# Optimization experiments

Measured on AMD Instinct MI355X. Metric: run time of the kernel, lower is better.

The kernel has to match this reference:

```python
import jax, jax.numpy as jnp
import numpy as np

B, D, K, NCLS, BANK = 1024, 256, 8, 71, 32


def setup_inputs() -> dict:
    key = jax.random.key(0)
    ks = jax.random.split(key, 8)
    p = lambda k: jax.random.normal(k, (D, D), jnp.float32) * 0.02  # trunc_normal std=0.02 approx
    z = jnp.zeros((D,), jnp.float32)
    return {
        "target_token": jax.random.normal(ks[0], (B, D), jnp.float32),
        "fea_bank": jax.random.normal(ks[1], (NCLS, BANK, D), jnp.float32),
        "W_e1": p(ks[2]), "b_e1": z,
        "W_o1": p(ks[3]), "b_o1": z,
        "W_e2": p(ks[4]), "b_e2": z,
        "W_o2": p(ks[5]), "b_o2": z,
        "W_f1": p(ks[6]),
        "W_f2": p(ks[7]),
    }


def reference(target_token, fea_bank, W_e1, b_e1, W_o1, b_o1,
              W_e2, b_e2, W_o2, b_o2, W_f1, W_f2):
    lin = lambda x, W, b: x @ W.T + b  # torch nn.Linear convention

    # class-mean bank and euclidean cdist [B, NCLS]
    fea_mean = fea_bank.mean(axis=1)                              # [C, D]
    d2 = (jnp.sum(target_token ** 2, -1, keepdims=True)
          - 2.0 * target_token @ fea_mean.T
          + jnp.sum(fea_mean ** 2, -1))
    dist = jnp.sqrt(jnp.maximum(d2, 0.0))
    _, idx = jax.lax.top_k(-dist, K)                              # k smallest -> [B, K]

    # stage 1: blend with nearest class means
    nearest_means = fea_mean[idx]                                 # [B, K, D]
    e1 = jax.nn.gelu(lin(nearest_means - target_token[:, None], W_e1, b_e1),
                     approximate=False)
    w1 = e1 @ W_f1.T
    e1 = e1 * jax.nn.softmax(w1, axis=1)                          # softmax over K
    off1 = jnp.tanh(lin(target_token[:, None] + e1, W_o1, b_o1))
    s1 = (1.0 + off1) * target_token[:, None]                     # [B, K, D]

    # stage 2: blend with full intra-class banks of selected classes
    feats = fea_bank[idx]                                         # [B, K, BANK, D]
    e2 = jax.nn.gelu(lin(feats - s1[:, :, None], W_e2, b_e2), approximate=False)
    w2 = e2 @ W_f2.T
    e2 = e2 * jax.nn.softmax(w2, axis=2)                          # softmax over BANK
    off2 = jnp.tanh(lin(s1[:, :, None] + e2, W_o2, b_o2))
    s2 = ((1.0 + off2) * s1[:, :, None]).sum(axis=2)              # [B, K, D]

    return (s1, s2)
```

## Files before the change

kernel.cpp:

```cpp
#include <hip/hip_runtime.h>
#include <hip/hip_bf16.h>

#define BB 1024
#define DD 256
#define KK 8
#define NCLS_ 71
#define BANK_ 32
#define BKROWS (BB*KK)
#define NBROWS (NCLS_*BANK_)

typedef __bf16 bf16x8 __attribute__((ext_vector_type(8)));
typedef __bf16 bf16x4 __attribute__((ext_vector_type(4)));
typedef float f32x4 __attribute__((ext_vector_type(4)));

__device__ __forceinline__ float gelu_fast(float x) {
    float z = __expf(-1.702f * x);
    return x * __builtin_amdgcn_rcpf(1.0f + z);
}
__device__ __forceinline__ float tanh_fast(float y) {
    float z = __expf(2.0f * y);
    return 1.0f - 2.0f * __builtin_amdgcn_rcpf(z + 1.0f);
}
__device__ __forceinline__ int swz(int row, int colByte) {
    return (row * 512 + colByte) ^ ((row & 7) << 4);
}

template<int MT, int NT>
__device__ __forceinline__ void gemm_tile(const __bf16* __restrict__ Wg,
                                          const char* Ab, int m_base, int n_base,
                                          int lane, f32x4 (&acc)[MT][NT])
{
    #pragma unroll
    for (int ks = 0; ks < 8; ++ks) {
        bf16x8 a[MT];
        #pragma unroll
        for (int mt = 0; mt < MT; ++mt) {
            int row = m_base + mt*16 + (lane & 15);
            int cb  = ks*64 + ((lane >> 4) << 4);
            a[mt] = *reinterpret_cast<const bf16x8*>(Ab + swz(row, cb));
        }
        #pragma unroll
        for (int nt = 0; nt < NT; ++nt) {
            int n  = n_base + nt*16 + (lane & 15);
            int k0 = ks*32 + ((lane >> 4) << 3);
            bf16x8 b = *reinterpret_cast<const bf16x8*>(Wg + n*DD + k0);
            #pragma unroll
            for (int mt = 0; mt < MT; ++mt)
                acc[mt][nt] = __builtin_amdgcn_mfma_f32_16x16x32_bf16(a[mt], b, acc[mt][nt], 0, 0, 0);
        }
    }
}

__global__ __launch_bounds__(256) void k_prep(
    const float* __restrict__ We1f, const float* __restrict__ Wo1f,
    const float* __restrict__ We2f, const float* __restrict__ Wo2f,
    const float* __restrict__ Wf1f, const float* __restrict__ Wf2f,
    const float* __restrict__ fb,
    __bf16* __restrict__ We1, __bf16* __restrict__ Wo1,
    __bf16* __restrict__ We2, __bf16* __restrict__ Wo2,
    __bf16* __restrict__ Wf1, __bf16* __restrict__ Wf2,
    __bf16* __restrict__ fbb, float* __restrict__ fmean)
{
    int b = blockIdx.x, tid = threadIdx.x;
    if (b < 384) {
        int w = b >> 6;
        const float* s; __bf16* d;
        switch (w) {
            case 0: s = We1f; d = We1; break;
            case 1: s = Wo1f; d = Wo1; break;
            case 2: s = We2f; d = We2; break;
            case 3: s = Wo2f; d = Wo2; break;
            case 4: s = Wf1f; d = Wf1; break;
            default: s = Wf2f; d = Wf2; break;
        }
        int i = (b & 63)*256 + tid;
        float4 v = reinterpret_cast<const float4*>(s)[i];
        bf16x4 o = {(__bf16)v.x, (__bf16)v.y, (__bf16)v.z, (__bf16)v.w};
        *reinterpret_cast<bf16x4*>(d + i*4) = o;
    } else if (b < 952) {
        int i = (b - 384)*256 + tid;
        float4 v = reinterpret_cast<const float4*>(fb)[i];
        bf16x4 o = {(__bf16)v.x, (__bf16)v.y, (__bf16)v.z, (__bf16)v.w};
        *reinterpret_cast<bf16x4*>(fbb + i*4) = o;
    } else {
        int c = b - 952, d = tid;
        float s = 0.f;
        #pragma unroll
        for (int j = 0; j < BANK_; ++j) s += fb[(c*BANK_ + j)*DD + d];
        fmean[c*DD + d] = s * (1.0f / BANK_);
    }
}

__global__ __launch_bounds__(64) void k_topk(const float* __restrict__ tgt,
                                             const float* __restrict__ fmean,
                                             int* __restrict__ idx) {
    __shared__ float d2s[NCLS_];
    int b = blockIdx.x, l = threadIdx.x;
    float t0 = tgt[b*DD + l],       t1 = tgt[b*DD + 64 + l];
    float t2 = tgt[b*DD + 128 + l], t3 = tgt[b*DD + 192 + l];
    for (int c = 0; c < NCLS_; ++c) {
        const float* m = fmean + c*DD;
        float a0 = t0 - m[l], a1 = t1 - m[64+l], a2 = t2 - m[128+l], a3 = t3 - m[192+l];
        float p = a0*a0 + a1*a1 + a2*a2 + a3*a3;
        #pragma unroll
        for (int o = 32; o > 0; o >>= 1) p += __shfl_xor(p, o);
        if (l == 0) d2s[c] = p;
    }
    if (l == 0) {
        for (int t = 0; t < KK; ++t) {
            float best = 3.4e38f; int bi = 0;
            for (int c = 0; c < NCLS_; ++c) { float v = d2s[c]; if (v < best) { best = v; bi = c; } }
            d2s[bi] = 3.4e38f;
            idx[b*KK + t] = bi;
        }
    }
}

__global__ __launch_bounds__(128) void k_stage1(
    const float* __restrict__ tgt, const float* __restrict__ fmean, const int* __restrict__ idx,
    const __bf16* __restrict__ We1, const float* __restrict__ be1,
    const __bf16* __restrict__ Wf1,
    const __bf16* __restrict__ Wo1, const float* __restrict__ bo1,
    float* __restrict__ out_s1, __bf16* __restrict__ s1b)
{
    __shared__ __bf16 As[16*256];
    __shared__ float tl[256];
    __shared__ int cls[8];
    char* Ab = (char*)As;
    int tid = threadIdx.x, lane = tid & 63, wid = tid >> 6;
    int b = blockIdx.x;
    if (tid < 8) cls[tid] = idx[b*KK + tid];
    if (tid < 64) reinterpret_cast<float4*>(tl)[tid] = reinterpret_cast<const float4*>(tgt + b*DD)[tid];
    {
        uint4 zz = {0u,0u,0u,0u};
        #pragma unroll
        for (int i = 0; i < 2; ++i) {
            int f = i*128 + tid;
            int row = 8 + (f >> 5), c = f & 31;
            *reinterpret_cast<uint4*>(Ab + swz(row, c*16)) = zz;
        }
    }
    __syncthreads();
    int c16 = tid & 31, q = tid >> 5;
    #pragma unroll
    for (int i = 0; i < 2; ++i) {
        int row = i*4 + q;
        const float* mb = fmean + cls[row]*DD + c16*8;
        const float* tb = tl + c16*8;
        float4 m0 = *(const float4*)mb, m1 = *(const float4*)(mb+4);
        float4 t0 = *(const float4*)tb, t1 = *(const float4*)(tb+4);
        bf16x8 o = {(__bf16)(m0.x-t0.x), (__bf16)(m0.y-t0.y), (__bf16)(m0.z-t0.z), (__bf16)(m0.w-t0.w),
                    (__bf16)(m1.x-t1.x), (__bf16)(m1.y-t1.y), (__bf16)(m1.z-t1.z), (__bf16)(m1.w-t1.w)};
        *reinterpret_cast<bf16x8*>(Ab + swz(row, c16*16)) = o;
    }
    __syncthreads();
    int n_base = wid * 128;
    int qr = lane >> 4;
    const f32x4 z = {0.f, 0.f, 0.f, 0.f};
    f32x4 acc[1][8];
    #pragma unroll
    for (int nt = 0; nt < 8; ++nt) acc[0][nt] = z;
    gemm_tile<1,8>(We1, Ab, 0, n_base, lane, acc);
    float e1reg[8][4];
    #pragma unroll
    for (int nt = 0; nt < 8; ++nt)
        #pragma unroll
        for (int r = 0; r < 4; ++r) {
            int col = n_base + nt*16 + (lane & 15);
            e1reg[nt][r] = gelu_fast(acc[0][nt][r] + be1[col]);
        }
    __syncthreads();
    if (qr < 2)
        #pragma unroll
        for (int nt = 0; nt < 8; ++nt)
            #pragma unroll
            for (int r = 0; r < 4; ++r) {
                int row = qr*4 + r;
                int col = n_base + nt*16 + (lane & 15);
                *(__bf16*)(Ab + swz(row, col*2)) = (__bf16)e1reg[nt][r];
            }
    __syncthreads();
    f32x4 acc2[1][8];
    #pragma unroll
    for (int nt = 0; nt < 8; ++nt) acc2[0][nt] = z;
    gemm_tile<1,8>(Wf1, Ab, 0, n_base, lane, acc2);
    float a2v[8][4];
    #pragma unroll
    for (int nt = 0; nt < 8; ++nt) {
        float mx = fmaxf(fmaxf(acc2[0][nt][0], acc2[0][nt][1]),
                         fmaxf(acc2[0][nt][2], acc2[0][nt][3]));
        mx = fmaxf(mx, __shfl_xor(mx, 16));
        float p[4], s = 0.f;
        #pragma unroll
        for (int r = 0; r < 4; ++r) { p[r] = __expf(acc2[0][nt][r] - mx); s += p[r]; }
        s += __shfl_xor(s, 16);
        float inv = __builtin_amdgcn_rcpf(s);
        int col = n_base + nt*16 + (lane & 15);
        #pragma unroll
        for (int r = 0; r < 4; ++r)
            a2v[nt][r] = tl[col] + e1reg[nt][r] * p[r] * inv;
    }
    __syncthreads();
    if (qr < 2)
        #pragma unroll
        for (int nt = 0; nt < 8; ++nt)
            #pragma unroll
            for (int r = 0; r < 4; ++r) {
                int row = qr*4 + r;
                int col = n_base + nt*16 + (lane & 15);
                *(__bf16*)(Ab + swz(row, col*2)) = (__bf16)a2v[nt][r];
            }
    __syncthreads();
    #pragma unroll
    for (int nt = 0; nt < 8; ++nt) acc[0][nt] = z;
    gemm_tile<1,8>(Wo1, Ab, 0, n_base, lane, acc);
    if (qr < 2)
        #pragma unroll
        for (int nt = 0; nt < 8; ++nt)
            #pragma unroll
            for (int r = 0; r < 4; ++r) {
                int row = qr*4 + r;
                int col = n_base + nt*16 + (lane & 15);
                float off = tanh_fast(acc[0][nt][r] + bo1[col]);
                float s1v = (1.0f + off) * tl[col];
                int g = (b*8 + row)*DD + col;
                out_s1[g] = s1v;
                s1b[g] = (__bf16)s1v;
            }
}

__global__ __launch_bounds__(256) void k_gemms(
    const __bf16* __restrict__ fbb, const __bf16* __restrict__ s1b,
    const __bf16* __restrict__ We2, const __bf16* __restrict__ Wo2,
    const float* __restrict__ be2, const float* __restrict__ bo2,
    float* __restrict__ FBe2b, float* __restrict__ S1We2, float* __restrict__ S1Wo2)
{
    __shared__ __bf16 As[64*256];
    char* Ab = (char*)As;
    int tid = threadIdx.x, lane = tid & 63, wid = tid >> 6;
    bool fbpath = blockIdx.x < 36;
    const __bf16* A = fbpath ? fbb : s1b;
    int m0 = fbpath ? blockIdx.x * 64 : (blockIdx.x - 36) * 64;
    int M  = fbpath ? NBROWS : BKROWS;
    #pragma unroll
    for (int i = 0; i < 8; ++i) {
        int f = i*256 + tid;
        int row = f >> 5, c16 = f & 31;
        uint4 v = {0u,0u,0u,0u};
        if (m0 + row < M) v = *reinterpret_cast<const uint4*>(A + (size_t)(m0+row)*DD + c16*8);
        *reinterpret_cast<uint4*>(Ab + swz(row, c16*16)) = v;
    }
    __syncthreads();
    int m_base = (wid >> 1) * 32, n_base = (wid & 1) * 128;
    const f32x4 z = {0.f, 0.f, 0.f, 0.f};
    f32x4 acc[2][8];
    #pragma unroll
    for (int mt = 0; mt < 2; ++mt)
        #pragma unroll
        for (int nt = 0; nt < 8; ++nt) acc[mt][nt] = z;
    gemm_tile<2,8>(We2, Ab, m_base, n_base, lane, acc);
    #pragma unroll
    for (int mt = 0; mt < 2; ++mt)
        #pragma unroll
        for (int nt = 0; nt < 8; ++nt)
            #pragma unroll
            for (int r = 0; r < 4; ++r) {
                int row = m_base + mt*16 + ((lane >> 4) << 2) + r;
                int col = n_base + nt*16 + (lane & 15);
                if (m0 + row < M) {
                    if (fbpath) FBe2b[(size_t)(m0+row)*DD + col] = acc[mt][nt][r] + be2[col];
                    else        S1We2[(size_t)(m0+row)*DD + col] = acc[mt][nt][r];
                }
            }
    if (!fbpath) {
        #pragma unroll
        for (int mt = 0; mt < 2; ++mt)
            #pragma unroll
            for (int nt = 0; nt < 8; ++nt) acc[mt][nt] = z;
        gemm_tile<2,8>(Wo2, Ab, m_base, n_base, lane, acc);
        #pragma unroll
        for (int mt = 0; mt < 2; ++mt)
            #pragma unroll
            for (int nt = 0; nt < 8; ++nt)
                #pragma unroll
                for (int r = 0; r < 4; ++r) {
                    int row = m_base + mt*16 + ((lane >> 4) << 2) + r;
                    int col = n_base + nt*16 + (lane & 15);
                    S1Wo2[(size_t)(m0+row)*DD + col] = acc[mt][nt][r] + bo2[col];
                }
    }
}

__global__ __launch_bounds__(512, 4) void k_stage2(
    const int* __restrict__ idx,
    const float* __restrict__ FBe2b,
    const float* __restrict__ S1We2,
    const float* __restrict__ S1Wo2,
    const __bf16* __restrict__ Wf2,
    const __bf16* __restrict__ Wo2,
    const float* __restrict__ s1,
    float* __restrict__ s2)
{
    __shared__ __bf16 As[128*256];
    __shared__ int clss[4];
    char* Ab = (char*)As;
    int tid = threadIdx.x, lane = tid & 63, wid = tid >> 6;
    int u0 = blockIdx.x * 4;
    if (tid < 4) clss[tid] = idx[u0 + tid];
    __syncthreads();
    int c16 = tid & 31, q = tid >> 5;
    #pragma unroll
    for (int i = 0; i < 8; ++i) {
        int row = i*16 + q;
        int unit = row >> 5, j = row & 31;
        const float* fbp = FBe2b + ((size_t)clss[unit]*BANK_ + j)*DD + c16*8;
        const float* sbp = S1We2 + (size_t)(u0+unit)*DD + c16*8;
        float4 f0 = *(const float4*)fbp, f1 = *(const float4*)(fbp+4);
        float4 g0 = *(const float4*)sbp, g1 = *(const float4*)(sbp+4);
        bf16x8 o = {(__bf16)gelu_fast(f0.x-g0.x), (__bf16)gelu_fast(f0.y-g0.y),
                    (__bf16)gelu_fast(f0.z-g0.z), (__bf16)gelu_fast(f0.w-g0.w),
                    (__bf16)gelu_fast(f1.x-g1.x), (__bf16)gelu_fast(f1.y-g1.y),
                    (__bf16)gelu_fast(f1.z-g1.z), (__bf16)gelu_fast(f1.w-g1.w)};
        *reinterpret_cast<bf16x8*>(Ab + swz(row, c16*16)) = o;
    }
    __syncthreads();
    int n_base = wid * 32;
    const f32x4 z = {0.f, 0.f, 0.f, 0.f};
    f32x4 acc[8][2];
    #pragma unroll
    for (int mt = 0; mt < 8; ++mt)
        #pragma unroll
        for (int nt = 0; nt < 2; ++nt) acc[mt][nt] = z;
    gemm_tile<8,2>(Wf2, Ab, 0, n_base, lane, acc);
    float inv_[4][2];
    #pragma unroll
    for (int unit = 0; unit < 4; ++unit)
        #pragma unroll
        for (int nt = 0; nt < 2; ++nt) {
            float mx = -3.4e38f;
            #pragma unroll
            for (int mh = 0; mh < 2; ++mh)
                #pragma unroll
                for (int r = 0; r < 4; ++r) mx = fmaxf(mx, acc[unit*2+mh][nt][r]);
            mx = fmaxf(mx, __shfl_xor(mx, 16));
            mx = fmaxf(mx, __shfl_xor(mx, 32));
            float s = 0.f;
            #pragma unroll
            for (int mh = 0; mh < 2; ++mh)
                #pragma unroll
                for (int r = 0; r < 4; ++r) {
                    float e = __expf(acc[unit*2+mh][nt][r] - mx);
                    acc[unit*2+mh][nt][r] = e;
                    s += e;
                }
            s += __shfl_xor(s, 16);
            s += __shfl_xor(s, 32);
            inv_[unit][nt] = __builtin_amdgcn_rcpf(s);
        }
    __syncthreads();
    #pragma unroll
    for (int mt = 0; mt < 8; ++mt)
        #pragma unroll
        for (int nt = 0; nt < 2; ++nt)
            #pragma unroll
            for (int r = 0; r < 4; ++r) {
                int row = mt*16 + ((lane >> 4) << 2) + r;
                int col = n_base + nt*16 + (lane & 15);
                __bf16* p16 = (__bf16*)(Ab + swz(row, col*2));
                *p16 = (__bf16)((float)*p16 * acc[mt][nt][r] * inv_[mt>>1][nt]);
            }
    __syncthreads();
    #pragma unroll
    for (int mt = 0; mt < 8; ++mt)
        #pragma unroll
        for (int nt = 0; nt < 2; ++nt) acc[mt][nt] = z;
    gemm_tile<8,2>(Wo2, Ab, 0, n_base, lane, acc);
    #pragma unroll
    for (int unit = 0; unit < 4; ++unit) {
        size_t u = u0 + unit;
        #pragma unroll
        for (int nt = 0; nt < 2; ++nt) {
            int col = n_base + nt*16 + (lane & 15);
            float srow = S1Wo2[u*DD + col];
            float cs = 0.f;
            #pragma unroll
            for (int mh = 0; mh < 2; ++mh)
                #pragma unroll
                for (int r = 0; r < 4; ++r) cs += tanh_fast(acc[unit*2+mh][nt][r] + srow);
            cs += __shfl_xor(cs, 16);
            cs += __shfl_xor(cs, 32);
            if ((lane >> 4) == 0)
                s2[u*DD + col] = s1[u*DD + col] * (32.0f + cs);
        }
    }
}

extern "C" void kernel_launch(void* const* d_in, const int* in_sizes, int n_in,
                              void* d_out, int out_size, void* d_ws, size_t ws_size,
                              hipStream_t stream)
{
    const float* tgt  = (const float*)d_in[0];
    const float* fb   = (const float*)d_in[1];
    const float* We1f = (const float*)d_in[2];
    const float* be1  = (const float*)d_in[3];
    const float* Wo1f = (const float*)d_in[4];
    const float* bo1  = (const float*)d_in[5];
    const float* We2f = (const float*)d_in[6];
    const float* be2  = (const float*)d_in[7];
    const float* Wo2f = (const float*)d_in[8];
    const float* bo2  = (const float*)d_in[9];
    const float* Wf1f = (const float*)d_in[10];
    const float* Wf2f = (const float*)d_in[11];

    char* ws = (char*)d_ws;
    size_t off = 0;
    auto alloc = [&](size_t bytes) { char* p = ws + off; off += (bytes + 255) & ~255ull; return p; };
    float*  fmean = (float*)alloc(NCLS_*DD*4);
    int*    idx   = (int*)alloc(BB*KK*4);
    __bf16* We1   = (__bf16*)alloc(DD*DD*2);
    __bf16* Wo1   = (__bf16*)alloc(DD*DD*2);
    __bf16* We2   = (__bf16*)alloc(DD*DD*2);
    __bf16* Wo2   = (__bf16*)alloc(DD*DD*2);
    __bf16* Wf1   = (__bf16*)alloc(DD*DD*2);
    __bf16* Wf2   = (__bf16*)alloc(DD*DD*2);
    __bf16* fbb   = (__bf16*)alloc((size_t)NBROWS*DD*2);
    __bf16* s1b   = (__bf16*)alloc((size_t)BKROWS*DD*2);
    float*  FBe2b = (float*)alloc((size_t)NBROWS*DD*4);
    float*  S1We2 = (float*)alloc((size_t)BKROWS*DD*4);
    float*  S1Wo2 = (float*)alloc((size_t)BKROWS*DD*4);

    float* out_s1 = (float*)d_out;
    float* out_s2 = out_s1 + (size_t)BKROWS*DD;

    k_prep<<<1023, 256, 0, stream>>>(We1f, Wo1f, We2f, Wo2f, Wf1f, Wf2f, fb,
                                     We1, Wo1, We2, Wo2, Wf1, Wf2, fbb, fmean);
    k_topk<<<BB, 64, 0, stream>>>(tgt, fmean, idx);
    k_stage1<<<BB, 128, 0, stream>>>(tgt, fmean, idx, We1, be1, Wf1, Wo1, bo1, out_s1, s1b);
    k_gemms<<<36 + BKROWS/64, 256, 0, stream>>>(fbb, s1b, We2, Wo2, be2, bo2,
                                                FBe2b, S1We2, S1Wo2);
    k_stage2<<<BKROWS/4, 512, 0, stream>>>(idx, FBe2b, S1We2, S1Wo2, Wf2, Wo2, out_s1, out_s2);
}
```

Before: 300.9 us.

## Fuse top-k into stage1, store intermediates as bf16, shrink gemm and stage2 tiles

```diff
diff --git a/kernel.cpp b/kernel.cpp
--- a/kernel.cpp
+++ b/kernel.cpp
@@ -91,53 +91,54 @@
     }
 }
 
-__global__ __launch_bounds__(64) void k_topk(const float* __restrict__ tgt,
-                                             const float* __restrict__ fmean,
-                                             int* __restrict__ idx) {
-    __shared__ float d2s[NCLS_];
-    int b = blockIdx.x, l = threadIdx.x;
-    float t0 = tgt[b*DD + l],       t1 = tgt[b*DD + 64 + l];
-    float t2 = tgt[b*DD + 128 + l], t3 = tgt[b*DD + 192 + l];
-    for (int c = 0; c < NCLS_; ++c) {
-        const float* m = fmean + c*DD;
-        float a0 = t0 - m[l], a1 = t1 - m[64+l], a2 = t2 - m[128+l], a3 = t3 - m[192+l];
-        float p = a0*a0 + a1*a1 + a2*a2 + a3*a3;
-        #pragma unroll
-        for (int o = 32; o > 0; o >>= 1) p += __shfl_xor(p, o);
-        if (l == 0) d2s[c] = p;
-    }
-    if (l == 0) {
+__global__ __launch_bounds__(128) void k_stage1(
+    const float* __restrict__ tgt, const float* __restrict__ fmean,
+    int* __restrict__ idxg,
+    const __bf16* __restrict__ We1, const float* __restrict__ be1,
+    const __bf16* __restrict__ Wf1,
+    const __bf16* __restrict__ Wo1, const float* __restrict__ bo1,
+    float* __restrict__ out_s1, __bf16* __restrict__ s1b)
+{
+    __shared__ __bf16 As[16*256];
+    __shared__ float tl[256];
+    __shared__ float d2s[NCLS_ + 1];
+    __shared__ int cls[8];
+    char* Ab = (char*)As;
+    int tid = threadIdx.x, lane = tid & 63, wid = tid >> 6;
+    int b = blockIdx.x;
+    if (tid < 64) reinterpret_cast<float4*>(tl)[tid] = reinterpret_cast<const float4*>(tgt + b*DD)[tid];
+    {
+        uint4 zz = {0u,0u,0u,0u};
+        #pragma unroll
+        for (int i = 0; i < 2; ++i) {
+            int f = i*128 + tid;
+            int row = 8 + (f >> 5), c = f & 31;
+            *reinterpret_cast<uint4*>(Ab + swz(row, c*16)) = zz;
+        }
+    }
+    __syncthreads();
+    {
+        float t0 = tl[lane], t1 = tl[64+lane], t2 = tl[128+lane], t3 = tl[192+lane];
+        int cbeg = wid*36, cend = cbeg + 36 - wid;
+        for (int c = cbeg; c < cend; ++c) {
+            const float* m = fmean + c*DD;
+            float a0 = t0 - m[lane], a1 = t1 - m[64+lane];
+            float a2 = t2 - m[128+lane], a3 = t3 - m[192+lane];
+            float p = a0*a0 + a1*a1 + a2*a2 + a3*a3;
+            #pragma unroll
+            for (int o = 32; o > 0; o >>= 1) p += __shfl_xor(p, o);
+            if (lane == 0) d2s[c] = p;
+        }
+    }
+    __syncthreads();
+    if (tid == 0) {
+        #pragma unroll
         for (int t = 0; t < KK; ++t) {
             float best = 3.4e38f; int bi = 0;
             for (int c = 0; c < NCLS_; ++c) { float v = d2s[c]; if (v < best) { best = v; bi = c; } }
             d2s[bi] = 3.4e38f;
-            idx[b*KK + t] = bi;
-        }
-    }
-}
-
-__global__ __launch_bounds__(128) void k_stage1(
-    const float* __restrict__ tgt, const float* __restrict__ fmean, const int* __restrict__ idx,
-    const __bf16* __restrict__ We1, const float* __restrict__ be1,
-    const __bf16* __restrict__ Wf1,
-    const __bf16* __restrict__ Wo1, const float* __restrict__ bo1,
-    float* __restrict__ out_s1, __bf16* __restrict__ s1b)
-{
-    __shared__ __bf16 As[16*256];
-    __shared__ float tl[256];
-    __shared__ int cls[8];
-    char* Ab = (char*)As;
-    int tid = threadIdx.x, lane = tid & 63, wid = tid >> 6;
-    int b = blockIdx.x;
-    if (tid < 8) cls[tid] = idx[b*KK + tid];
-    if (tid < 64) reinterpret_cast<float4*>(tl)[tid] = reinterpret_cast<const float4*>(tgt + b*DD)[tid];
-    {
-        uint4 zz = {0u,0u,0u,0u};
-        #pragma unroll
-        for (int i = 0; i < 2; ++i) {
-            int f = i*128 + tid;
-            int row = 8 + (f >> 5), c = f & 31;
-            *reinterpret_cast<uint4*>(Ab + swz(row, c*16)) = zz;
+            cls[t] = bi;
+            idxg[b*KK + t] = bi;
         }
     }
     __syncthreads();
@@ -233,108 +234,100 @@
     const __bf16* __restrict__ fbb, const __bf16* __restrict__ s1b,
     const __bf16* __restrict__ We2, const __bf16* __restrict__ Wo2,
     const float* __restrict__ be2, const float* __restrict__ bo2,
-    float* __restrict__ FBe2b, float* __restrict__ S1We2, float* __restrict__ S1Wo2)
-{
-    __shared__ __bf16 As[64*256];
+    __bf16* __restrict__ FBe2b, __bf16* __restrict__ S1We2, __bf16* __restrict__ S1Wo2)
+{
+    __shared__ __bf16 As[32*256];
     char* Ab = (char*)As;
     int tid = threadIdx.x, lane = tid & 63, wid = tid >> 6;
-    bool fbpath = blockIdx.x < 36;
+    bool fbpath = blockIdx.x < 71;
     const __bf16* A = fbpath ? fbb : s1b;
-    int m0 = fbpath ? blockIdx.x * 64 : (blockIdx.x - 36) * 64;
-    int M  = fbpath ? NBROWS : BKROWS;
-    #pragma unroll
-    for (int i = 0; i < 8; ++i) {
+    int m0 = fbpath ? blockIdx.x * 32 : (blockIdx.x - 71) * 32;
+    #pragma unroll
+    for (int i = 0; i < 4; ++i) {
         int f = i*256 + tid;
         int row = f >> 5, c16 = f & 31;
-        uint4 v = {0u,0u,0u,0u};
-        if (m0 + row < M) v = *reinterpret_cast<const uint4*>(A + (size_t)(m0+row)*DD + c16*8);
+        uint4 v = *reinterpret_cast<const uint4*>(A + (size_t)(m0+row)*DD + c16*8);
         *reinterpret_cast<uint4*>(Ab + swz(row, c16*16)) = v;
     }
     __syncthreads();
-    int m_base = (wid >> 1) * 32, n_base = (wid & 1) * 128;
+    int n_base = wid * 64;
     const f32x4 z = {0.f, 0.f, 0.f, 0.f};
-    f32x4 acc[2][8];
+    f32x4 acc[2][4];
     #pragma unroll
     for (int mt = 0; mt < 2; ++mt)
         #pragma unroll
-        for (int nt = 0; nt < 8; ++nt) acc[mt][nt] = z;
-    gemm_tile<2,8>(We2, Ab, m_base, n_base, lane, acc);
+        for (int nt = 0; nt < 4; ++nt) acc[mt][nt] = z;
+    gemm_tile<2,4>(We2, Ab, 0, n_base, lane, acc);
     #pragma unroll
     for (int mt = 0; mt < 2; ++mt)
         #pragma unroll
-        for (int nt = 0; nt < 8; ++nt)
+        for (int nt = 0; nt < 4; ++nt)
             #pragma unroll
             for (int r = 0; r < 4; ++r) {
-                int row = m_base + mt*16 + ((lane >> 4) << 2) + r;
+                int row = mt*16 + ((lane >> 4) << 2) + r;
                 int col = n_base + nt*16 + (lane & 15);
-                if (m0 + row < M) {
-                    if (fbpath) FBe2b[(size_t)(m0+row)*DD + col] = acc[mt][nt][r] + be2[col];
-                    else        S1We2[(size_t)(m0+row)*DD + col] = acc[mt][nt][r];
-                }
+                if (fbpath) FBe2b[(size_t)(m0+row)*DD + col] = (__bf16)(acc[mt][nt][r] + be2[col]);
+                else        S1We2[(size_t)(m0+row)*DD + col] = (__bf16)acc[mt][nt][r];
             }
     if (!fbpath) {
         #pragma unroll
         for (int mt = 0; mt < 2; ++mt)
             #pragma unroll
-            for (int nt = 0; nt < 8; ++nt) acc[mt][nt] = z;
-        gemm_tile<2,8>(Wo2, Ab, m_base, n_base, lane, acc);
+            for (int nt = 0; nt < 4; ++nt) acc[mt][nt] = z;
+        gemm_tile<2,4>(Wo2, Ab, 0, n_base, lane, acc);
         #pragma unroll
         for (int mt = 0; mt < 2; ++mt)
             #pragma unroll
-            for (int nt = 0; nt < 8; ++nt)
+            for (int nt = 0; nt < 4; ++nt)
                 #pragma unroll
                 for (int r = 0; r < 4; ++r) {
-                    int row = m_base + mt*16 + ((lane >> 4) << 2) + r;
+                    int row = mt*16 + ((lane >> 4) << 2) + r;
                     int col = n_base + nt*16 + (lane & 15);
-                    S1Wo2[(size_t)(m0+row)*DD + col] = acc[mt][nt][r] + bo2[col];
+                    S1Wo2[(size_t)(m0+row)*DD + col] = (__bf16)(acc[mt][nt][r] + bo2[col]);
                 }
     }
 }
 
 __global__ __launch_bounds__(512, 4) void k_stage2(
     const int* __restrict__ idx,
-    const float* __restrict__ FBe2b,
-    const float* __restrict__ S1We2,
-    const float* __restrict__ S1Wo2,
+    const __bf16* __restrict__ FBe2b,
+    const __bf16* __restrict__ S1We2,
+    const __bf16* __restrict__ S1Wo2,
     const __bf16* __restrict__ Wf2,
     const __bf16* __restrict__ Wo2,
     const float* __restrict__ s1,
     float* __restrict__ s2)
 {
-    __shared__ __bf16 As[128*256];
-    __shared__ int clss[4];
+    __shared__ __bf16 As[64*256];
     char* Ab = (char*)As;
     int tid = threadIdx.x, lane = tid & 63, wid = tid >> 6;
-    int u0 = blockIdx.x * 4;
-    if (tid < 4) clss[tid] = idx[u0 + tid];
-    __syncthreads();
+    int u0 = blockIdx.x * 2;
+    int cls0 = idx[u0], cls1 = idx[u0+1];
     int c16 = tid & 31, q = tid >> 5;
     #pragma unroll
-    for (int i = 0; i < 8; ++i) {
+    for (int i = 0; i < 4; ++i) {
         int row = i*16 + q;
         int unit = row >> 5, j = row & 31;
-        const float* fbp = FBe2b + ((size_t)clss[unit]*BANK_ + j)*DD + c16*8;
-        const float* sbp = S1We2 + (size_t)(u0+unit)*DD + c16*8;
-        float4 f0 = *(const float4*)fbp, f1 = *(const float4*)(fbp+4);
-        float4 g0 = *(const float4*)sbp, g1 = *(const float4*)(sbp+4);
-        bf16x8 o = {(__bf16)gelu_fast(f0.x-g0.x), (__bf16)gelu_fast(f0.y-g0.y),
-                    (__bf16)gelu_fast(f0.z-g0.z), (__bf16)gelu_fast(f0.w-g0.w),
-                    (__bf16)gelu_fast(f1.x-g1.x), (__bf16)gelu_fast(f1.y-g1.y),
-                    (__bf16)gelu_fast(f1.z-g1.z), (__bf16)gelu_fast(f1.w-g1.w)};
+        int cls = unit ? cls1 : cls0;
+        bf16x8 f = *reinterpret_cast<const bf16x8*>(FBe2b + ((size_t)cls*BANK_ + j)*DD + c16*8);
+        bf16x8 g = *reinterpret_cast<const bf16x8*>(S1We2 + (size_t)(u0+unit)*DD + c16*8);
+        bf16x8 o;
+        #pragma unroll
+        for (int e = 0; e < 8; ++e) o[e] = (__bf16)gelu_fast((float)f[e] - (float)g[e]);
         *reinterpret_cast<bf16x8*>(Ab + swz(row, c16*16)) = o;
     }
     __syncthreads();
     int n_base = wid * 32;
     const f32x4 z = {0.f, 0.f, 0.f, 0.f};
-    f32x4 acc[8][2];
-    #pragma unroll
-    for (int mt = 0; mt < 8; ++mt)
+    f32x4 acc[4][2];
+    #pragma unroll
+    for (int mt = 0; mt < 4; ++mt)
         #pragma unroll
         for (int nt = 0; nt < 2; ++nt) acc[mt][nt] = z;
-    gemm_tile<8,2>(Wf2, Ab, 0, n_base, lane, acc);
-    float inv_[4][2];
-    #pragma unroll
-    for (int unit = 0; unit < 4; ++unit)
+    gemm_tile<4,2>(Wf2, Ab, 0, n_base, lane, acc);
+    float inv_[2][2];
+    #pragma unroll
+    for (int unit = 0; unit < 2; ++unit)
         #pragma unroll
         for (int nt = 0; nt < 2; ++nt) {
             float mx = -3.4e38f;
@@ -359,7 +352,7 @@
         }
     __syncthreads();
     #pragma unroll
-    for (int mt = 0; mt < 8; ++mt)
+    for (int mt = 0; mt < 4; ++mt)
         #pragma unroll
         for (int nt = 0; nt < 2; ++nt)
             #pragma unroll
@@ -371,17 +364,17 @@
             }
     __syncthreads();
     #pragma unroll
-    for (int mt = 0; mt < 8; ++mt)
+    for (int mt = 0; mt < 4; ++mt)
         #pragma unroll
         for (int nt = 0; nt < 2; ++nt) acc[mt][nt] = z;
-    gemm_tile<8,2>(Wo2, Ab, 0, n_base, lane, acc);
-    #pragma unroll
-    for (int unit = 0; unit < 4; ++unit) {
+    gemm_tile<4,2>(Wo2, Ab, 0, n_base, lane, acc);
+    #pragma unroll
+    for (int unit = 0; unit < 2; ++unit) {
         size_t u = u0 + unit;
         #pragma unroll
         for (int nt = 0; nt < 2; ++nt) {
             int col = n_base + nt*16 + (lane & 15);
-            float srow = S1Wo2[u*DD + col];
+            float srow = (float)S1Wo2[u*DD + col];
             float cs = 0.f;
             #pragma unroll
             for (int mh = 0; mh < 2; ++mh)
@@ -425,18 +418,17 @@
     __bf16* Wf2   = (__bf16*)alloc(DD*DD*2);
     __bf16* fbb   = (__bf16*)alloc((size_t)NBROWS*DD*2);
     __bf16* s1b   = (__bf16*)alloc((size_t)BKROWS*DD*2);
-    float*  FBe2b = (float*)alloc((size_t)NBROWS*DD*4);
-    float*  S1We2 = (float*)alloc((size_t)BKROWS*DD*4);
-    float*  S1Wo2 = (float*)alloc((size_t)BKROWS*DD*4);
+    __bf16* FBe2b = (__bf16*)alloc((size_t)NBROWS*DD*2);
+    __bf16* S1We2 = (__bf16*)alloc((size_t)BKROWS*DD*2);
+    __bf16* S1Wo2 = (__bf16*)alloc((size_t)BKROWS*DD*2);
 
     float* out_s1 = (float*)d_out;
     float* out_s2 = out_s1 + (size_t)BKROWS*DD;
 
     k_prep<<<1023, 256, 0, stream>>>(We1f, Wo1f, We2f, Wo2f, Wf1f, Wf2f, fb,
                                      We1, Wo1, We2, Wo2, Wf1, Wf2, fbb, fmean);
-    k_topk<<<BB, 64, 0, stream>>>(tgt, fmean, idx);
     k_stage1<<<BB, 128, 0, stream>>>(tgt, fmean, idx, We1, be1, Wf1, Wo1, bo1, out_s1, s1b);
-    k_gemms<<<36 + BKROWS/64, 256, 0, stream>>>(fbb, s1b, We2, Wo2, be2, bo2,
+    k_gemms<<<71 + BKROWS/32, 256, 0, stream>>>(fbb, s1b, We2, Wo2, be2, bo2,
                                                 FBe2b, S1We2, S1Wo2);
-    k_stage2<<<BKROWS/4, 512, 0, stream>>>(idx, FBe2b, S1We2, S1Wo2, Wf2, Wo2, out_s1, out_s2);
-}
+    k_stage2<<<BKROWS/2, 512, 0, stream>>>(idx, FBe2b, S1We2, S1Wo2, Wf2, Wo2, out_s1, out_s2);
+}
```

New measurement: 260.7 us. 13.4% less time.
